# Performance work log

Measured on AMD Instinct MI355X. Metric: run time of the kernel, lower is better.

Reference implementation:

```python
import jax, jax.numpy as jnp
import numpy as np

N_NODES = 100000
N_EDGES = 2500000
N_GRAPHS = 1024


def setup_inputs() -> dict:
    key = jax.random.key(0)
    ks = jax.random.split(key, 12)
    inp = {
        "x": jax.random.normal(ks[0], (N_NODES, 7), dtype=jnp.float32),
        "e": jax.random.uniform(ks[1], (N_EDGES,), dtype=jnp.float32),
        "W1": jax.random.normal(ks[2], (7, 32), dtype=jnp.float32) * 0.3,
        "b1": jnp.zeros((32,), dtype=jnp.float32),
        "W2": jax.random.normal(ks[3], (32, 32), dtype=jnp.float32) * 0.2,
        "b2": jnp.zeros((32,), dtype=jnp.float32),
        "W3": jax.random.normal(ks[4], (32, 32), dtype=jnp.float32) * 0.2,
        "b3": jnp.zeros((32,), dtype=jnp.float32),
        "W4": jax.random.normal(ks[5], (32, 2), dtype=jnp.float32) * 0.2,
        "b4": jnp.zeros((2,), dtype=jnp.float32),
        "src": jax.random.randint(ks[6], (N_EDGES,), 0, N_NODES, dtype=jnp.int32),
        "dst": jax.random.randint(ks[7], (N_EDGES,), 0, N_NODES, dtype=jnp.int32),
        "graph_id": jnp.sort(jax.random.randint(ks[8], (N_NODES,), 0, N_GRAPHS, dtype=jnp.int32)),
        "n_graphs": N_GRAPHS,
    }
    return inp


def _graph_conv(feat, W, b, src, dst, norm_out, norm_in, edge_weight=None):
    # DGL GraphConv, norm='both': D_out^{-1/2} -> (weighted) sum aggregation -> D_in^{-1/2} -> linear
    n = feat.shape[0]
    h = feat * norm_out[:, None]
    m = h[src]  # [E, d] gather
    if edge_weight is not None:
        m = m * edge_weight[:, None]
    agg = jax.ops.segment_sum(m, dst, num_segments=n)  # [N, d]
    agg = agg * norm_in[:, None]
    return agg @ W + b


def reference(x, e, W1, b1, W2, b2, W3, b3, W4, b4, src, dst, graph_id, n_graphs):
    n = x.shape[0]
    ones_e = jnp.ones((src.shape[0],), dtype=x.dtype)
    deg_out = jax.ops.segment_sum(ones_e, src, num_segments=n)
    deg_in = jax.ops.segment_sum(ones_e, dst, num_segments=n)
    norm_out = jax.lax.rsqrt(jnp.clip(deg_out, 1.0))  # degs.clamp(min=1)^{-1/2}
    norm_in = jax.lax.rsqrt(jnp.clip(deg_in, 1.0))

    h = jax.nn.relu(_graph_conv(x, W1, b1, src, dst, norm_out, norm_in, edge_weight=e))
    h = jax.nn.relu(_graph_conv(h, W2, b2, src, dst, norm_out, norm_in))
    h = jax.nn.relu(_graph_conv(h, W3, b3, src, dst, norm_out, norm_in))
    h = _graph_conv(h, W4, b4, src, dst, norm_out, norm_in)

    # dgl.mean_nodes: per-graph mean of node features
    sums = jax.ops.segment_sum(h, graph_id, num_segments=n_graphs)  # [G, 2]
    cnts = jax.ops.segment_sum(jnp.ones((n,), dtype=h.dtype), graph_id, num_segments=n_graphs)
    return sums / jnp.clip(cnts, 1.0)[:, None]
```

## Files before the change

kernel.cpp:

```cpp
#include <hip/hip_runtime.h>

#define NN 100000
#define NE 2500000
#define BK_SHIFT 7
#define BK_NODES 128
#define NBUCK ((NN + BK_NODES - 1) / BK_NODES)
#define TILE 4096
#define NTILES ((NE + TILE - 1) / TILE)
#define SRC_MASK 0x1FFFF


__global__ __launch_bounds__(256) void k_tilecnt2(const int* __restrict__ src,
                                                  const int* __restrict__ dst,
                                                  int* __restrict__ tot_d, int* __restrict__ tot_s,
                                                  int E) {
    __shared__ int cd[NBUCK];
    __shared__ int cs[NBUCK];
    int base = blockIdx.x * TILE;
    for (int i = threadIdx.x; i < NBUCK; i += 256) { cd[i] = 0; cs[i] = 0; }
    __syncthreads();
#pragma unroll
    for (int k = 0; k < 16; ++k) {
        int idx = base + threadIdx.x + k * 256;
        if (idx < E) {
            atomicAdd(&cd[dst[idx] >> BK_SHIFT], 1);
            atomicAdd(&cs[src[idx] >> BK_SHIFT], 1);
        }
    }
    __syncthreads();
    for (int i = threadIdx.x; i < NBUCK; i += 256) {
        int c = cd[i]; if (c) atomicAdd(&tot_d[i], c);
        c = cs[i];     if (c) atomicAdd(&tot_s[i], c);
    }
}

__global__ __launch_bounds__(1024) void k_bucket_scan(const int* __restrict__ tot_d,
                                                      const int* __restrict__ tot_s,
                                                      int* __restrict__ base_d, int* __restrict__ base_s,
                                                      int* __restrict__ cursor_d, int* __restrict__ cursor_s,
                                                      int* __restrict__ row_ptr, int E) {
    __shared__ int sh[1024];
    int tid = threadIdx.x;
    int v = (tid < NBUCK) ? tot_d[tid] : 0;
    sh[tid] = v;
    __syncthreads();
#pragma unroll
    for (int off = 1; off < 1024; off <<= 1) {
        int t = (tid >= off) ? sh[tid - off] : 0;
        __syncthreads();
        sh[tid] += t;
        __syncthreads();
    }
    if (tid < NBUCK) { int ex = sh[tid] - v; base_d[tid] = ex; cursor_d[tid] = ex; }
    if (tid == 0) { base_d[NBUCK] = E; row_ptr[NN] = E; }
    __syncthreads();
    v = (tid < NBUCK) ? tot_s[tid] : 0;
    sh[tid] = v;
    __syncthreads();
#pragma unroll
    for (int off = 1; off < 1024; off <<= 1) {
        int t = (tid >= off) ? sh[tid - off] : 0;
        __syncthreads();
        sh[tid] += t;
        __syncthreads();
    }
    if (tid < NBUCK) { int ex = sh[tid] - v; base_s[tid] = ex; cursor_s[tid] = ex; }
    if (tid == 0) base_s[NBUCK] = E;
}

__global__ __launch_bounds__(256) void k_binpass2(
    const int* __restrict__ src, const int* __restrict__ dst, const float* __restrict__ ew,
    int* __restrict__ cursor_d, int* __restrict__ cursor_s,
    int2* __restrict__ stage2, unsigned char* __restrict__ stage_s, int E) {
    __shared__ int cnt_d[NBUCK];
    __shared__ int gpos_d[NBUCK];
    __shared__ int cnt_s[NBUCK];
    __shared__ int gpos_s[NBUCK];

    int base = blockIdx.x * TILE;
    for (int i = threadIdx.x; i < NBUCK; i += 256) { cnt_d[i] = 0; cnt_s[i] = 0; }
    __syncthreads();

    int w0[16]; float w1[16]; int pd[16]; int rs[16];
#pragma unroll
    for (int k = 0; k < 16; ++k) {
        int idx = base + threadIdx.x + k * 256;
        pd[k] = -1;
        if (idx < E) {
            int s = src[idx], d = dst[idx];
            w1[k] = ew[idx];
            int bd = d >> BK_SHIFT;
            w0[k] = s | ((d & (BK_NODES - 1)) << 17);
            int rd = atomicAdd(&cnt_d[bd], 1);
            pd[k] = bd | (rd << 10);
            rs[k] = atomicAdd(&cnt_s[s >> BK_SHIFT], 1);
        }
    }
    __syncthreads();

    for (int i = threadIdx.x; i < NBUCK; i += 256) {
        int c = cnt_d[i]; if (c) gpos_d[i] = atomicAdd(&cursor_d[i], c);
        c = cnt_s[i];     if (c) gpos_s[i] = atomicAdd(&cursor_s[i], c);
    }
    __syncthreads();

#pragma unroll
    for (int k = 0; k < 16; ++k) {
        if (pd[k] >= 0) {
            int bd = pd[k] & 1023, rd = pd[k] >> 10;
            stage2[gpos_d[bd] + rd] = make_int2(w0[k], __float_as_int(w1[k]));
            int s = w0[k] & SRC_MASK;
            stage_s[gpos_s[s >> BK_SHIFT] + rs[k]] = (unsigned char)(s & (BK_NODES - 1));
        }
    }
}

__global__ __launch_bounds__(256) void k_prep_src(
    const int* __restrict__ base_s, const unsigned char* __restrict__ stage_s, const float* __restrict__ x,
    float* __restrict__ no, float* __restrict__ xs, int N) {
    __shared__ int cnt[BK_NODES];
    int b = blockIdx.x;
    int beg = base_s[b], end = base_s[b + 1];
    if (threadIdx.x < BK_NODES) cnt[threadIdx.x] = 0;
    __syncthreads();
    for (int j = beg + threadIdx.x; j < end; j += 256) atomicAdd(&cnt[stage_s[j]], 1);
    __syncthreads();
    if (threadIdx.x < BK_NODES) {
        int n = (b << BK_SHIFT) + threadIdx.x;
        if (n < N) {
            float nov = rsqrtf(fmaxf((float)cnt[threadIdx.x], 1.0f));
            no[n] = nov;
#pragma unroll
            for (int f = 0; f < 7; ++f) xs[n * 8 + f] = x[n * 7 + f] * nov;
            xs[n * 8 + 7] = 0.f;
        }
    }
}

__global__ __launch_bounds__(256) void k_scatter2(
    const int* __restrict__ base_d, const int2* __restrict__ stage2,
    int* __restrict__ row_ptr, float* __restrict__ ni,
    int* __restrict__ csr_src, float* __restrict__ csr_w, int N) {
    __shared__ int cnt[BK_NODES];
    __shared__ int scn[BK_NODES];
    __shared__ int cur[BK_NODES];
    int b = blockIdx.x;
    int beg = base_d[b], end = base_d[b + 1];
    if (threadIdx.x < BK_NODES) cnt[threadIdx.x] = 0;
    __syncthreads();
    for (int j = beg + threadIdx.x; j < end; j += 256) atomicAdd(&cnt[stage2[j].x >> 17], 1);
    __syncthreads();
    int v = (threadIdx.x < BK_NODES) ? cnt[threadIdx.x] : 0;
    if (threadIdx.x < BK_NODES) scn[threadIdx.x] = v;
    __syncthreads();
#pragma unroll
    for (int off = 1; off < BK_NODES; off <<= 1) {
        int t = (threadIdx.x < BK_NODES && threadIdx.x >= off) ? scn[threadIdx.x - off] : 0;
        __syncthreads();
        if (threadIdx.x < BK_NODES) scn[threadIdx.x] += t;
        __syncthreads();
    }
    if (threadIdx.x < BK_NODES) {
        int ex = scn[threadIdx.x] - v;
        cur[threadIdx.x] = beg + ex;
        int n = (b << BK_SHIFT) + threadIdx.x;
        if (n < N) {
            row_ptr[n] = beg + ex;
            ni[n] = rsqrtf(fmaxf((float)v, 1.0f));
        }
    }
    __syncthreads();
    for (int j = beg + threadIdx.x; j < end; j += 256) {
        int2 t = stage2[j];
        int dl = t.x >> 17;
        int pos = atomicAdd(&cur[dl], 1);
        csr_src[pos] = t.x & SRC_MASK;
        csr_w[pos] = __int_as_float(t.y);
    }
}


__global__ __launch_bounds__(256) void k_layer1(
    const int* __restrict__ rp, const int* __restrict__ csr_src, const float* __restrict__ csr_w,
    const float* __restrict__ xs, const float* __restrict__ ni, const float* __restrict__ no,
    const float* __restrict__ W1, const float* __restrict__ b1, float* __restrict__ h1s, int N) {
    __shared__ float sW[7 * 32];
    __shared__ float sb[32];
    __shared__ float sh7[32][8];
    for (int i = threadIdx.x; i < 7 * 32; i += 256) sW[i] = W1[i];
    if (threadIdx.x < 32) sb[threadIdx.x] = b1[threadIdx.x];

    int g = threadIdx.x >> 3, lane = threadIdx.x & 7;
    int node = blockIdx.x * 32 + g;
    float acc = 0.f;
    if (node < N) {
        int beg = rp[node], end = rp[node + 1];
        for (int j0 = beg; j0 < end; j0 += 8) {
            int ms = 0; float mw = 0.f;
            if (j0 + lane < end) {
                ms = csr_src[j0 + lane];
                mw = csr_w[j0 + lane];
            }
            int m = end - j0; if (m > 8) m = 8;
            float a0 = 0.f, a1 = 0.f, a2 = 0.f, a3 = 0.f;
            int k = 0;
            for (; k + 4 <= m; k += 4) {
                int s0 = __shfl(ms, k, 8);     float w0 = __shfl(mw, k, 8);
                int s1 = __shfl(ms, k + 1, 8); float w1 = __shfl(mw, k + 1, 8);
                int s2 = __shfl(ms, k + 2, 8); float w2 = __shfl(mw, k + 2, 8);
                int s3 = __shfl(ms, k + 3, 8); float w3 = __shfl(mw, k + 3, 8);
                a0 += xs[s0 * 8 + lane] * w0;
                a1 += xs[s1 * 8 + lane] * w1;
                a2 += xs[s2 * 8 + lane] * w2;
                a3 += xs[s3 * 8 + lane] * w3;
            }
            for (; k < m; ++k) {
                int s = __shfl(ms, k, 8);
                float w = __shfl(mw, k, 8);
                a0 += xs[s * 8 + lane] * w;
            }
            acc += (a0 + a1) + (a2 + a3);
        }
        acc *= ni[node];
    }
    sh7[g][lane] = acc;
    __syncthreads();

    int g2 = threadIdx.x >> 5, l32 = threadIdx.x & 31;
#pragma unroll
    for (int t = 0; t < 4; ++t) {
        int nl = t * 8 + g2;
        int node2 = blockIdx.x * 32 + nl;
        if (node2 < N) {
            float o = sb[l32];
#pragma unroll
            for (int k = 0; k < 7; ++k) o += sh7[nl][k] * sW[k * 32 + l32];
            h1s[node2 * 32 + l32] = fmaxf(o, 0.f) * no[node2];
        }
    }
}

__global__ __launch_bounds__(256) void k_layer32(
    const int* __restrict__ rp, const int* __restrict__ csr_src, const float* __restrict__ h_in,
    const float* __restrict__ ni, const float* __restrict__ no, const float* __restrict__ W,
    const float* __restrict__ b, float* __restrict__ h_out, int N) {
    __shared__ float sW[32 * 32];
    __shared__ float sb[32];
    __shared__ float shv[8][32];
    for (int i = threadIdx.x; i < 1024; i += 256) sW[i] = W[i];
    if (threadIdx.x < 32) sb[threadIdx.x] = b[threadIdx.x];

    int g = threadIdx.x >> 5, lane = threadIdx.x & 31;
    int node = blockIdx.x * 8 + g;
    float acc = 0.f;
    if (node < N) {
        int beg = rp[node], end = rp[node + 1];
        for (int j0 = beg; j0 < end; j0 += 32) {
            int ms = (j0 + lane < end) ? csr_src[j0 + lane] : 0;
            int m = end - j0; if (m > 32) m = 32;
            float a0 = 0.f, a1 = 0.f, a2 = 0.f, a3 = 0.f;
            int k = 0;
            for (; k + 4 <= m; k += 4) {
                int s0 = __shfl(ms, k, 32);
                int s1 = __shfl(ms, k + 1, 32);
                int s2 = __shfl(ms, k + 2, 32);
                int s3 = __shfl(ms, k + 3, 32);
                a0 += h_in[s0 * 32 + lane];
                a1 += h_in[s1 * 32 + lane];
                a2 += h_in[s2 * 32 + lane];
                a3 += h_in[s3 * 32 + lane];
            }
            for (; k < m; ++k) {
                int s = __shfl(ms, k, 32);
                a0 += h_in[s * 32 + lane];
            }
            acc += (a0 + a1) + (a2 + a3);
        }
        acc *= ni[node];
    }
    shv[g][lane] = acc;
    __syncthreads();
    if (node < N) {
        float o = sb[lane];
#pragma unroll
        for (int k = 0; k < 32; ++k) o += shv[g][k] * sW[k * 32 + lane];
        h_out[node * 32 + lane] = fmaxf(o, 0.f) * no[node];
    }
}

__global__ __launch_bounds__(256) void k_layer34(
    const int* __restrict__ rp, const int* __restrict__ csr_src, const float* __restrict__ h_in,
    const float* __restrict__ ni, const float* __restrict__ no, const float* __restrict__ W3,
    const float* __restrict__ b3, const float* __restrict__ W4, float2* __restrict__ h4pre, int N) {
    __shared__ float sW[32 * 32];
    __shared__ float sb[32];
    __shared__ float sW4[64];
    __shared__ float shv[8][32];
    for (int i = threadIdx.x; i < 1024; i += 256) sW[i] = W3[i];
    if (threadIdx.x < 32) sb[threadIdx.x] = b3[threadIdx.x];
    if (threadIdx.x < 64) sW4[threadIdx.x] = W4[threadIdx.x];

    int g = threadIdx.x >> 5, lane = threadIdx.x & 31;
    int node = blockIdx.x * 8 + g;
    float acc = 0.f;
    if (node < N) {
        int beg = rp[node], end = rp[node + 1];
        for (int j0 = beg; j0 < end; j0 += 32) {
            int ms = (j0 + lane < end) ? csr_src[j0 + lane] : 0;
            int m = end - j0; if (m > 32) m = 32;
            float a0 = 0.f, a1 = 0.f, a2 = 0.f, a3 = 0.f;
            int k = 0;
            for (; k + 4 <= m; k += 4) {
                int s0 = __shfl(ms, k, 32);
                int s1 = __shfl(ms, k + 1, 32);
                int s2 = __shfl(ms, k + 2, 32);
                int s3 = __shfl(ms, k + 3, 32);
                a0 += h_in[s0 * 32 + lane];
                a1 += h_in[s1 * 32 + lane];
                a2 += h_in[s2 * 32 + lane];
                a3 += h_in[s3 * 32 + lane];
            }
            for (; k < m; ++k) {
                int s = __shfl(ms, k, 32);
                a0 += h_in[s * 32 + lane];
            }
            acc += (a0 + a1) + (a2 + a3);
        }
        acc *= ni[node];
    }
    shv[g][lane] = acc;
    __syncthreads();
    if (node < N) {
        float o = sb[lane];
#pragma unroll
        for (int k = 0; k < 32; ++k) o += shv[g][k] * sW[k * 32 + lane];
        float t = fmaxf(o, 0.f) * no[node];
        float px = t * sW4[lane * 2 + 0];
        float py = t * sW4[lane * 2 + 1];
#pragma unroll
        for (int off = 16; off; off >>= 1) {
            px += __shfl_xor(px, off, 32);
            py += __shfl_xor(py, off, 32);
        }
        if (lane == 0) h4pre[node] = make_float2(px, py);
    }
}

__global__ void k_agg4(const int* __restrict__ rp, const int* __restrict__ csr_src,
                       const float2* __restrict__ h4pre, const float* __restrict__ ni,
                       float2* __restrict__ agg2, int N) {
    int n = blockIdx.x * blockDim.x + threadIdx.x;
    if (n >= N) return;
    int beg = rp[n], end = rp[n + 1];
    float ax0 = 0.f, ay0 = 0.f, ax1 = 0.f, ay1 = 0.f;
    int j = beg;
    for (; j + 2 <= end; j += 2) {
        int s0 = csr_src[j], s1 = csr_src[j + 1];
        float2 v0 = h4pre[s0];
        float2 v1 = h4pre[s1];
        ax0 += v0.x; ay0 += v0.y;
        ax1 += v1.x; ay1 += v1.y;
    }
    if (j < end) {
        float2 v = h4pre[csr_src[j]];
        ax0 += v.x; ay0 += v.y;
    }
    float w = ni[n];
    agg2[n] = make_float2((ax0 + ax1) * w, (ay0 + ay1) * w);
}

__global__ void k_pool(const float2* __restrict__ agg2, const int* __restrict__ gid,
                       const float* __restrict__ b4, float* __restrict__ out, int N) {
    int g = blockIdx.x;
    int lo = 0, hi = N;
    while (lo < hi) { int m = (lo + hi) >> 1; if (gid[m] < g) lo = m + 1; else hi = m; }
    int start = lo;
    int lo2 = start, hi2 = N;
    while (lo2 < hi2) { int m = (lo2 + hi2) >> 1; if (gid[m] < g + 1) lo2 = m + 1; else hi2 = m; }
    int end = lo2;
    float sx = 0.f, sy = 0.f;
    for (int n = start + threadIdx.x; n < end; n += 64) {
        float2 v = agg2[n];
        sx += v.x;
        sy += v.y;
    }
#pragma unroll
    for (int off = 32; off; off >>= 1) {
        sx += __shfl_down(sx, off, 64);
        sy += __shfl_down(sy, off, 64);
    }
    if (threadIdx.x == 0) {
        int cnt = end - start;
        float inv = 1.0f / fmaxf((float)cnt, 1.0f);
        float scale = (float)cnt * inv;
        out[g * 2 + 0] = sx * inv + b4[0] * scale;
        out[g * 2 + 1] = sy * inv + b4[1] * scale;
    }
}


extern "C" void kernel_launch(void* const* d_in, const int* in_sizes, int n_in,
                              void* d_out, int out_size, void* d_ws, size_t ws_size,
                              hipStream_t stream) {
    const float* x   = (const float*)d_in[0];
    const float* e   = (const float*)d_in[1];
    const float* W1  = (const float*)d_in[2];
    const float* b1  = (const float*)d_in[3];
    const float* W2  = (const float*)d_in[4];
    const float* b2  = (const float*)d_in[5];
    const float* W3  = (const float*)d_in[6];
    const float* b3  = (const float*)d_in[7];
    const float* W4  = (const float*)d_in[8];
    const float* b4  = (const float*)d_in[9];
    const int*   src = (const int*)d_in[10];
    const int*   dst = (const int*)d_in[11];
    const int*   gid = (const int*)d_in[12];
    float* out = (float*)d_out;

    const int N = NN, E = NE;
    const int G = out_size / 2;

    int* ws_i = (int*)d_ws;
    int* tot_d    = ws_i;
    int* tot_s    = ws_i + 1024;
    int* base_d   = ws_i + 2048;
    int* base_s   = ws_i + 3072;
    int* cursor_d = ws_i + 4096;
    int* cursor_s = ws_i + 5120;
    int* row_ptr  = ws_i + 6144;
    int* csr_src  = ws_i + 6144 + (size_t)N + 4;
    float* csr_w  = (float*)(ws_i + 6144 + (size_t)N + 4 + (size_t)E);
    unsigned char* stage_s = (unsigned char*)csr_w;

    float* fbase = (float*)(ws_i + 6144 + (size_t)N + 4 + 2 * (size_t)E);
    float* no_b  = fbase;
    float* ni_b  = fbase + (size_t)N;
    float* xs    = fbase + (size_t)2 * N;
    float* h1s   = fbase + (size_t)10 * N;
    float* h2s   = fbase + (size_t)42 * N;
    float2* h4pre = (float2*)(fbase + (size_t)74 * N);
    float2* agg2  = (float2*)(fbase + (size_t)76 * N);
    int2* stage2 = (int2*)(fbase + (size_t)10 * N);

    hipMemsetAsync(ws_i, 0, 2048 * sizeof(int), stream);

    k_tilecnt2<<<NTILES, 256, 0, stream>>>(src, dst, tot_d, tot_s, E);
    k_bucket_scan<<<1, 1024, 0, stream>>>(tot_d, tot_s, base_d, base_s, cursor_d, cursor_s, row_ptr, E);
    k_binpass2<<<NTILES, 256, 0, stream>>>(src, dst, e, cursor_d, cursor_s, stage2, stage_s, E);
    k_prep_src<<<NBUCK, 256, 0, stream>>>(base_s, stage_s, x, no_b, xs, N);
    k_scatter2<<<NBUCK, 256, 0, stream>>>(base_d, stage2, row_ptr, ni_b, csr_src, csr_w, N);

    k_layer1<<<(N + 31) / 32, 256, 0, stream>>>(row_ptr, csr_src, csr_w, xs, ni_b, no_b, W1, b1, h1s, N);
    k_layer32<<<(N + 7) / 8, 256, 0, stream>>>(row_ptr, csr_src, h1s, ni_b, no_b, W2, b2, h2s, N);
    k_layer34<<<(N + 7) / 8, 256, 0, stream>>>(row_ptr, csr_src, h2s, ni_b, no_b, W3, b3, W4, h4pre, N);
    k_agg4<<<(N + 255) / 256, 256, 0, stream>>>(row_ptr, csr_src, h4pre, ni_b, agg2, N);
    k_pool<<<G, 64, 0, stream>>>(agg2, gid, b4, out, N);
}
```

Measured before the change: 439.6 us.

## Split hidden features into 8-wide column chunks and aggregate per chunk

Stores the 32-wide hidden features as four separate 8-float column planes, then runs the neighbor gather per chunk with an extra grid dimension, so each chunk table (3.2MB) fits better in cache. The fused aggregate+matmul kernels are split into a gather kernel and a separate dense matmul kernel. This adds extra kernel launches, writes and rereads of aggregated buffers, and re-reads the CSR indices four times per layer.

```diff
diff --git a/kernel.cpp b/kernel.cpp
--- a/kernel.cpp
+++ b/kernel.cpp
@@ -183,7 +183,7 @@
 __global__ __launch_bounds__(256) void k_layer1(
     const int* __restrict__ rp, const int* __restrict__ csr_src, const float* __restrict__ csr_w,
     const float* __restrict__ xs, const float* __restrict__ ni, const float* __restrict__ no,
-    const float* __restrict__ W1, const float* __restrict__ b1, float* __restrict__ h1s, int N) {
+    const float* __restrict__ W1, const float* __restrict__ b1, float* __restrict__ h1c, int N) {
     __shared__ float sW[7 * 32];
     __shared__ float sb[32];
     __shared__ float sh7[32][8];
@@ -235,63 +235,87 @@
             float o = sb[l32];
 #pragma unroll
             for (int k = 0; k < 7; ++k) o += sh7[nl][k] * sW[k * 32 + l32];
-            h1s[node2 * 32 + l32] = fmaxf(o, 0.f) * no[node2];
-        }
-    }
-}
-
-__global__ __launch_bounds__(256) void k_layer32(
-    const int* __restrict__ rp, const int* __restrict__ csr_src, const float* __restrict__ h_in,
-    const float* __restrict__ ni, const float* __restrict__ no, const float* __restrict__ W,
-    const float* __restrict__ b, float* __restrict__ h_out, int N) {
+            h1c[(size_t)(l32 >> 3) * N * 8 + (size_t)node2 * 8 + (l32 & 7)] =
+                fmaxf(o, 0.f) * no[node2];
+        }
+    }
+}
+
+__device__ __forceinline__ void proc8(int msr, int mm, const float* __restrict__ tbl, int lane,
+                                      float& a0, float& a1, float& a2, float& a3) {
+    if (mm >= 8) {
+        a0 += tbl[__shfl(msr, 0, 8) * 8 + lane];
+        a1 += tbl[__shfl(msr, 1, 8) * 8 + lane];
+        a2 += tbl[__shfl(msr, 2, 8) * 8 + lane];
+        a3 += tbl[__shfl(msr, 3, 8) * 8 + lane];
+        a0 += tbl[__shfl(msr, 4, 8) * 8 + lane];
+        a1 += tbl[__shfl(msr, 5, 8) * 8 + lane];
+        a2 += tbl[__shfl(msr, 6, 8) * 8 + lane];
+        a3 += tbl[__shfl(msr, 7, 8) * 8 + lane];
+    } else {
+        int kl = 0;
+        for (; kl + 4 <= mm; kl += 4) {
+            a0 += tbl[__shfl(msr, kl, 8) * 8 + lane];
+            a1 += tbl[__shfl(msr, kl + 1, 8) * 8 + lane];
+            a2 += tbl[__shfl(msr, kl + 2, 8) * 8 + lane];
+            a3 += tbl[__shfl(msr, kl + 3, 8) * 8 + lane];
+        }
+        for (; kl < mm; ++kl) a0 += tbl[__shfl(msr, kl, 8) * 8 + lane];
+    }
+}
+
+__global__ __launch_bounds__(256) void k_aggc(
+    const int* __restrict__ rp, const int* __restrict__ csr_src, const float* __restrict__ hc_in,
+    const float* __restrict__ ni, float* __restrict__ aggout, int N) {
+    int g = threadIdx.x >> 3, lane = threadIdx.x & 7;
+    int c = blockIdx.y;
+    int node = blockIdx.x * 32 + g;
+    if (node >= N) return;
+    const float* tbl = hc_in + (size_t)c * N * 8;
+    int beg = rp[node], end = rp[node + 1];
+    float acc = 0.f;
+    for (int j0 = beg; j0 < end; j0 += 32) {
+        int m = end - j0; if (m > 32) m = 32;
+        int ms0 = (j0 + lane < end) ? csr_src[j0 + lane] : 0;
+        int ms1 = (j0 + 8 + lane < end) ? csr_src[j0 + 8 + lane] : 0;
+        int ms2 = (j0 + 16 + lane < end) ? csr_src[j0 + 16 + lane] : 0;
+        int ms3 = (j0 + 24 + lane < end) ? csr_src[j0 + 24 + lane] : 0;
+        float a0 = 0.f, a1 = 0.f, a2 = 0.f, a3 = 0.f;
+        proc8(ms0, m, tbl, lane, a0, a1, a2, a3);
+        if (m > 8)  proc8(ms1, m - 8, tbl, lane, a0, a1, a2, a3);
+        if (m > 16) proc8(ms2, m - 16, tbl, lane, a0, a1, a2, a3);
+        if (m > 24) proc8(ms3, m - 24, tbl, lane, a0, a1, a2, a3);
+        acc += (a0 + a1) + (a2 + a3);
+    }
+    acc *= ni[node];
+    aggout[(size_t)c * N * 8 + (size_t)node * 8 + lane] = acc;
+}
+
+__global__ __launch_bounds__(256) void k_mm2(
+    const float* __restrict__ agg, const float* __restrict__ W, const float* __restrict__ bia,
+    const float* __restrict__ no, float* __restrict__ hc_out, int N) {
     __shared__ float sW[32 * 32];
     __shared__ float sb[32];
     __shared__ float shv[8][32];
     for (int i = threadIdx.x; i < 1024; i += 256) sW[i] = W[i];
-    if (threadIdx.x < 32) sb[threadIdx.x] = b[threadIdx.x];
-
+    if (threadIdx.x < 32) sb[threadIdx.x] = bia[threadIdx.x];
     int g = threadIdx.x >> 5, lane = threadIdx.x & 31;
-    int node = blockIdx.x * 8 + g;
-    float acc = 0.f;
-    if (node < N) {
-        int beg = rp[node], end = rp[node + 1];
-        for (int j0 = beg; j0 < end; j0 += 32) {
-            int ms = (j0 + lane < end) ? csr_src[j0 + lane] : 0;
-            int m = end - j0; if (m > 32) m = 32;
-            float a0 = 0.f, a1 = 0.f, a2 = 0.f, a3 = 0.f;
-            int k = 0;
-            for (; k + 4 <= m; k += 4) {
-                int s0 = __shfl(ms, k, 32);
-                int s1 = __shfl(ms, k + 1, 32);
-                int s2 = __shfl(ms, k + 2, 32);
-                int s3 = __shfl(ms, k + 3, 32);
-                a0 += h_in[s0 * 32 + lane];
-                a1 += h_in[s1 * 32 + lane];
-                a2 += h_in[s2 * 32 + lane];
-                a3 += h_in[s3 * 32 + lane];
-            }
-            for (; k < m; ++k) {
-                int s = __shfl(ms, k, 32);
-                a0 += h_in[s * 32 + lane];
-            }
-            acc += (a0 + a1) + (a2 + a3);
-        }
-        acc *= ni[node];
-    }
-    shv[g][lane] = acc;
-    __syncthreads();
-    if (node < N) {
+    int n = blockIdx.x * 8 + g;
+    if (n < N)
+        shv[g][lane] = agg[(size_t)(lane >> 3) * N * 8 + (size_t)n * 8 + (lane & 7)];
+    __syncthreads();
+    if (n < N) {
         float o = sb[lane];
 #pragma unroll
         for (int k = 0; k < 32; ++k) o += shv[g][k] * sW[k * 32 + lane];
-        h_out[node * 32 + lane] = fmaxf(o, 0.f) * no[node];
-    }
-}
-
-__global__ __launch_bounds__(256) void k_layer34(
-    const int* __restrict__ rp, const int* __restrict__ csr_src, const float* __restrict__ h_in,
-    const float* __restrict__ ni, const float* __restrict__ no, const float* __restrict__ W3,
-    const float* __restrict__ b3, const float* __restrict__ W4, float2* __restrict__ h4pre, int N) {
+        hc_out[(size_t)(lane >> 3) * N * 8 + (size_t)n * 8 + (lane & 7)] =
+            fmaxf(o, 0.f) * no[n];
+    }
+}
+
+__global__ __launch_bounds__(256) void k_mm3(
+    const float* __restrict__ agg, const float* __restrict__ W3, const float* __restrict__ b3,
+    const float* __restrict__ W4, const float* __restrict__ no, float2* __restrict__ h4pre, int N) {
     __shared__ float sW[32 * 32];
     __shared__ float sb[32];
     __shared__ float sW4[64];
@@ -299,42 +323,16 @@
     for (int i = threadIdx.x; i < 1024; i += 256) sW[i] = W3[i];
     if (threadIdx.x < 32) sb[threadIdx.x] = b3[threadIdx.x];
     if (threadIdx.x < 64) sW4[threadIdx.x] = W4[threadIdx.x];
-
     int g = threadIdx.x >> 5, lane = threadIdx.x & 31;
-    int node = blockIdx.x * 8 + g;
-    float acc = 0.f;
-    if (node < N) {
-        int beg = rp[node], end = rp[node + 1];
-        for (int j0 = beg; j0 < end; j0 += 32) {
-            int ms = (j0 + lane < end) ? csr_src[j0 + lane] : 0;
-            int m = end - j0; if (m > 32) m = 32;
-            float a0 = 0.f, a1 = 0.f, a2 = 0.f, a3 = 0.f;
-            int k = 0;
-            for (; k + 4 <= m; k += 4) {
-                int s0 = __shfl(ms, k, 32);
-                int s1 = __shfl(ms, k + 1, 32);
-                int s2 = __shfl(ms, k + 2, 32);
-                int s3 = __shfl(ms, k + 3, 32);
-                a0 += h_in[s0 * 32 + lane];
-                a1 += h_in[s1 * 32 + lane];
-                a2 += h_in[s2 * 32 + lane];
-                a3 += h_in[s3 * 32 + lane];
-            }
-            for (; k < m; ++k) {
-                int s = __shfl(ms, k, 32);
-                a0 += h_in[s * 32 + lane];
-            }
-            acc += (a0 + a1) + (a2 + a3);
-        }
-        acc *= ni[node];
-    }
-    shv[g][lane] = acc;
-    __syncthreads();
-    if (node < N) {
+    int n = blockIdx.x * 8 + g;
+    if (n < N)
+        shv[g][lane] = agg[(size_t)(lane >> 3) * N * 8 + (size_t)n * 8 + (lane & 7)];
+    __syncthreads();
+    if (n < N) {
         float o = sb[lane];
 #pragma unroll
         for (int k = 0; k < 32; ++k) o += shv[g][k] * sW[k * 32 + lane];
-        float t = fmaxf(o, 0.f) * no[node];
+        float t = fmaxf(o, 0.f) * no[n];
         float px = t * sW4[lane * 2 + 0];
         float py = t * sW4[lane * 2 + 1];
 #pragma unroll
@@ -342,7 +340,7 @@
             px += __shfl_xor(px, off, 32);
             py += __shfl_xor(py, off, 32);
         }
-        if (lane == 0) h4pre[node] = make_float2(px, py);
+        if (lane == 0) h4pre[n] = make_float2(px, py);
     }
 }
 
@@ -436,11 +434,12 @@
     float* no_b  = fbase;
     float* ni_b  = fbase + (size_t)N;
     float* xs    = fbase + (size_t)2 * N;
-    float* h1s   = fbase + (size_t)10 * N;
-    float* h2s   = fbase + (size_t)42 * N;
+    float* h1c   = fbase + (size_t)10 * N;
+    float* h2c   = fbase + (size_t)42 * N;
     float2* h4pre = (float2*)(fbase + (size_t)74 * N);
     float2* agg2  = (float2*)(fbase + (size_t)76 * N);
     int2* stage2 = (int2*)(fbase + (size_t)10 * N);
+    float* agg3 = h1c;
 
     hipMemsetAsync(ws_i, 0, 2048 * sizeof(int), stream);
 
@@ -450,9 +449,12 @@
     k_prep_src<<<NBUCK, 256, 0, stream>>>(base_s, stage_s, x, no_b, xs, N);
     k_scatter2<<<NBUCK, 256, 0, stream>>>(base_d, stage2, row_ptr, ni_b, csr_src, csr_w, N);
 
-    k_layer1<<<(N + 31) / 32, 256, 0, stream>>>(row_ptr, csr_src, csr_w, xs, ni_b, no_b, W1, b1, h1s, N);
-    k_layer32<<<(N + 7) / 8, 256, 0, stream>>>(row_ptr, csr_src, h1s, ni_b, no_b, W2, b2, h2s, N);
-    k_layer34<<<(N + 7) / 8, 256, 0, stream>>>(row_ptr, csr_src, h2s, ni_b, no_b, W3, b3, W4, h4pre, N);
+    dim3 gAgg((N + 31) / 32, 4);
+    k_layer1<<<(N + 31) / 32, 256, 0, stream>>>(row_ptr, csr_src, csr_w, xs, ni_b, no_b, W1, b1, h1c, N);
+    k_aggc<<<gAgg, 256, 0, stream>>>(row_ptr, csr_src, h1c, ni_b, h2c, N);
+    k_mm2<<<(N + 7) / 8, 256, 0, stream>>>(h2c, W2, b2, no_b, h2c, N);
+    k_aggc<<<gAgg, 256, 0, stream>>>(row_ptr, csr_src, h2c, ni_b, agg3, N);
+    k_mm3<<<(N + 7) / 8, 256, 0, stream>>>(agg3, W3, b3, W4, no_b, h4pre, N);
     k_agg4<<<(N + 255) / 256, 256, 0, stream>>>(row_ptr, csr_src, h4pre, ni_b, agg2, N);
     k_pool<<<G, 64, 0, stream>>>(agg2, gid, b4, out, N);
 }
```

After: 469.9 us. 1.07x slower.
